# Optimization experiments

Measured on AMD Instinct MI355X. Metric: run time of the kernel, lower is better.

Reference implementation:

```python
import jax, jax.numpy as jnp
import numpy as np

H = 8      # num_heads
DH = 80    # head_dim = embed_dim // num_heads


def setup_inputs() -> dict:
    key = jax.random.key(0)
    ks = jax.random.split(key, 7)
    B, T, S = 8, 4096, 77
    hidden, embed, ctx = 640, 640, 768
    sc_h = 1.0 / np.sqrt(hidden)
    sc_c = 1.0 / np.sqrt(ctx)
    sc_e = 1.0 / np.sqrt(embed)
    return {
        "tokens": jax.random.normal(ks[0], (B, T, hidden), jnp.float32),
        "context": jax.random.normal(ks[1], (B, S, ctx), jnp.float32),
        "Wq": jax.random.normal(ks[2], (hidden, embed), jnp.float32) * sc_h,
        "Wk": jax.random.normal(ks[3], (ctx, embed), jnp.float32) * sc_c,
        "Wv": jax.random.normal(ks[4], (ctx, embed), jnp.float32) * sc_c,
        "Wo": jax.random.normal(ks[5], (embed, hidden), jnp.float32) * sc_e,
        "bo": jnp.zeros((hidden,), jnp.float32),
    }


def reference(tokens, context, Wq, Wk, Wv, Wo, bo):
    B, T, _ = tokens.shape
    S = context.shape[1]
    Q = (tokens @ Wq).reshape(B, T, H, DH)    # B T H D
    K = (context @ Wk).reshape(B, S, H, DH)   # B S H D
    V = (context @ Wv).reshape(B, S, H, DH)
    scores = jnp.einsum('bthd,bshd->bhts', Q, K) / jnp.sqrt(jnp.float32(DH))
    attn = jax.nn.softmax(scores, axis=-1)    # B H T S
    ctx_vecs = jnp.einsum('bhts,bshd->bthd', attn, V).reshape(B, T, H * DH)
    return ctx_vecs @ Wo + bo
```

## Files before the change

### kernel.cpp

```cpp
#include <hip/hip_runtime.h>
#include <hip/hip_bf16.h>
#include <hip/hip_fp16.h>

typedef __attribute__((ext_vector_type(4))) float f32x4;
typedef __attribute__((ext_vector_type(8))) _Float16 f16x8;
typedef __attribute__((ext_vector_type(8))) unsigned short u16x8;

__device__ __forceinline__ unsigned short f2h(float f) {
    _Float16 h = (_Float16)f;
    return __builtin_bit_cast(unsigned short, h);
}

#define GLOAD_LDS16(gp, lp) __builtin_amdgcn_global_load_lds( \
    (const __attribute__((address_space(1))) void*)(gp), \
    (__attribute__((address_space(3))) void*)(lp), 16, 0, 0)
#define PRIO1() __builtin_amdgcn_s_setprio(1)
#define PRIO0() __builtin_amdgcn_s_setprio(0)

__global__ void cvt_kernel(const float* __restrict__ in, ushort* __restrict__ out, int n4) {
    int stride = gridDim.x * blockDim.x;
    for (int i = blockIdx.x * blockDim.x + threadIdx.x; i < n4; i += stride) {
        float4 v = ((const float4*)in)[i];
        ushort4 o;
        o.x = f2h(v.x); o.y = f2h(v.y); o.z = f2h(v.z); o.w = f2h(v.w);
        ((ushort4*)out)[i] = o;
    }
}

__global__ void transpose_cvt2(const float* __restrict__ Wk, const float* __restrict__ Wv,
                               ushort* __restrict__ WkvT) {
    __shared__ float tile[32][33];
    const int z = blockIdx.z;
    const float* src = z ? Wv : Wk;
    ushort* dst = WkvT + (size_t)z * 640 * 768;
    const int R = 768, C = 640;
    int tx = threadIdx.x, ty = threadIdx.y;
    int c = blockIdx.x * 32 + tx;
    int r0 = blockIdx.y * 32;
#pragma unroll
    for (int i = ty; i < 32; i += 8) {
        int r = r0 + i;
        tile[i][tx] = (r < R && c < C) ? src[(size_t)r * C + c] : 0.f;
    }
    __syncthreads();
    int rr = r0 + tx;
    int c0 = blockIdx.x * 32;
#pragma unroll
    for (int i = ty; i < 32; i += 8) {
        int cc = c0 + i;
        if (cc < C && rr < R) dst[(size_t)cc * R + rr] = f2h(tile[tx][i]);
    }
}

__global__ void pack_wfrag(const float* __restrict__ W, ushort* __restrict__ WF) {
    int g = blockIdx.x * 256 + threadIdx.x;
    if (g >= 51200) return;
    int lane = g & 63;
    int fi = (g >> 6) % 10;
    int kt = ((g >> 6) / 10) % 10;
    int h  = (g >> 6) / 100;
    int ni = fi >> 1, kk = fi & 1;
    int n  = h * 80 + ni * 16 + (lane & 15);
    int k0 = kt * 64 + kk * 32 + (lane >> 4) * 8;
    u16x8 o;
#pragma unroll
    for (int e = 0; e < 8; ++e) o[e] = f2h(W[(size_t)(k0 + e) * 640 + n]);
    *(u16x8*)&WF[(size_t)g * 8] = o;
}

__global__ void pack_kvfrag(const ushort* __restrict__ KVb,
                            ushort* __restrict__ KF, ushort* __restrict__ VF) {
    int g = blockIdx.x * 256 + threadIdx.x;
    if (g >= 61440) return;
    int lane = g & 63;
    int fi = (g >> 6) % 15;
    int bh = (g >> 6) / 15;
    int b = bh >> 3, h = bh & 7;
    int ni = fi / 3, kk = fi % 3;
    int l15 = lane & 15, lhi = lane >> 4;
    int sr = ni * 16 + l15; if (sr > 76) sr = 76;
    int d0 = kk * 32 + lhi * 8;
    u16x8 ko, vo;
#pragma unroll
    for (int e = 0; e < 8; ++e)
        ko[e] = KVb[((size_t)b * 77 + sr) * 1280 + h * 80 + d0 + e];
    int dv = ni * 16 + l15;
    int s0 = kk * 32 + lhi * 8;
#pragma unroll
    for (int e = 0; e < 8; ++e) {
        int s = s0 + e;
        vo[e] = (s < 77) ? KVb[((size_t)b * 77 + s) * 1280 + 640 + h * 80 + dv] : (ushort)0;
    }
    *(u16x8*)&KF[(size_t)g * 8] = ko;
    *(u16x8*)&VF[(size_t)g * 8] = vo;
}

template<int OUT_F16, int HAS_BIAS>
__global__ __launch_bounds__(256) void gemm_bt(
    const ushort* __restrict__ A, const ushort* __restrict__ Bt,
    void* __restrict__ C, const float* __restrict__ bias,
    int M, int N, int K)
{
    __shared__ ushort As[128 * 64];
    __shared__ ushort Bs[128 * 64];
    const int tid = threadIdx.x;
    const int lane = tid & 63;
    const int w = tid >> 6;
    const int wr = (w >> 1) * 64, wc = (w & 1) * 64;
    const int m0 = blockIdx.x * 128, n0 = blockIdx.y * 128;
    const int l15 = lane & 15, lhi = lane >> 4;

    f32x4 acc[4][4] = {};

    for (int k0 = 0; k0 < K; k0 += 64) {
        __syncthreads();
#pragma unroll
        for (int i = 0; i < 4; ++i) {
            int c = i * 256 + tid;
            int m = m0 + (c >> 3);
            if (m > M - 1) m = M - 1;
            GLOAD_LDS16(A + (size_t)m * K + k0 + (c & 7) * 8, &As[c * 8]);
        }
#pragma unroll
        for (int i = 0; i < 4; ++i) {
            int c = i * 256 + tid;
            GLOAD_LDS16(Bt + (size_t)(n0 + (c >> 3)) * K + k0 + (c & 7) * 8, &Bs[c * 8]);
        }
        __syncthreads();
#pragma unroll
        for (int kk = 0; kk < 2; ++kk) {
            f16x8 af[4], bfr[4];
#pragma unroll
            for (int mi = 0; mi < 4; ++mi)
                af[mi] = *(const f16x8*)&As[(wr + mi * 16 + l15) * 64 + kk * 32 + lhi * 8];
#pragma unroll
            for (int ni = 0; ni < 4; ++ni)
                bfr[ni] = *(const f16x8*)&Bs[(wc + ni * 16 + l15) * 64 + kk * 32 + lhi * 8];
#pragma unroll
            for (int mi = 0; mi < 4; ++mi)
#pragma unroll
                for (int ni = 0; ni < 4; ++ni)
                    acc[mi][ni] = __builtin_amdgcn_mfma_f32_16x16x32_f16(
                        af[mi], bfr[ni], acc[mi][ni], 0, 0, 0);
        }
    }

#pragma unroll
    for (int mi = 0; mi < 4; ++mi)
#pragma unroll
        for (int ni = 0; ni < 4; ++ni)
#pragma unroll
            for (int r = 0; r < 4; ++r) {
                int row = m0 + wr + mi * 16 + lhi * 4 + r;
                int col = n0 + wc + ni * 16 + l15;
                if (row < M) {
                    float v = acc[mi][ni][r];
                    if (HAS_BIAS) v += bias[col];
                    if (OUT_F16) ((ushort*)C)[(size_t)row * N + col] = f2h(v);
                    else         ((float*)C)[(size_t)row * N + col] = v;
                }
            }
}

__global__ __launch_bounds__(1024, 1) void fused_attn(
    const float* __restrict__ tokens, const ushort* __restrict__ WqF,
    const ushort* __restrict__ KF, const ushort* __restrict__ VF,
    const ushort* __restrict__ WoF, const float* __restrict__ bo,
    float* __restrict__ out)
{
    __shared__ __align__(16) ushort lds[40960];
    const int tid = threadIdx.x;
    const int lane = tid & 63;
    const int w = tid >> 6;
    const int h = w & 7;
    const int rh = w >> 3;
    const int l15 = lane & 15, lhi = lane >> 4;
    const int tt = blockIdx.x, b = blockIdx.y;
    const size_t rowbase = (size_t)b * 4096 + (size_t)tt * 64;

    const ushort* WqFb = WqF + (size_t)h * 10 * 5120;
    const ushort* WoFb = WoF + (size_t)h * 10 * 5120;
    const ushort* KFb  = KF + (size_t)(b * 8 + h) * 15 * 512;
    const ushort* VFb  = VF + (size_t)(b * 8 + h) * 15 * 512;

    const bool stager = tid < 512;
    const int rs = (tid & 511) >> 3;
    const int ss = tid & 7;
    const int ds = rs * 64 + (ss ^ (rs & 7)) * 8;

#define STAGE_LOAD(C, A0, B0) do { \
    if (stager) { \
        const float* p_ = tokens + (rowbase + rs) * 640 + (C) * 64 + ss * 8; \
        A0 = ((const float4*)p_)[0]; B0 = ((const float4*)p_)[1]; \
    } \
} while (0)
#define STAGE_WRITE(BUF, A0, B0) do { \
    if (stager) { \
        u16x8 o_; \
        o_[0]=f2h(A0.x); o_[1]=f2h(A0.y); o_[2]=f2h(A0.z); o_[3]=f2h(A0.w); \
        o_[4]=f2h(B0.x); o_[5]=f2h(B0.y); o_[6]=f2h(B0.z); o_[7]=f2h(B0.w); \
        *(u16x8*)&lds[(BUF) * 4096 + ds] = o_; \
    } \
} while (0)

    {
        float4 a0, b0;
        STAGE_LOAD(0, a0, b0);
        STAGE_WRITE(0, a0, b0);
    }
    f16x8 PE[5], PO[5];
#pragma unroll
    for (int f = 0; f < 5; ++f)
        PE[f] = *(const f16x8*)(WqFb + (f * 2) * 512 + lane * 8);
    __syncthreads();

    f32x4 acc[2][5];
#define ZACC() do { \
    _Pragma("unroll") for (int i_ = 0; i_ < 2; ++i_) \
    _Pragma("unroll") for (int j_ = 0; j_ < 5; ++j_) \
        acc[i_][j_] = (f32x4){0.f, 0.f, 0.f, 0.f}; \
} while (0)

#define MHALF(PC, PN, WB, CURB, RSTR, SBASE, KK, NKT, NKK, DOPF) do { \
    if (DOPF) { \
        _Pragma("unroll") for (int f = 0; f < 5; ++f) \
            (PN)[f] = *(const f16x8*)((WB) + (size_t)(NKT) * 5120 + (f * 2 + (NKK)) * 512 + lane * 8); \
    } \
    PRIO1(); \
    _Pragma("unroll") for (int mi = 0; mi < 2; ++mi) { \
        int row_ = rh * 32 + mi * 16 + l15; \
        f16x8 a_ = *(const f16x8*)&lds[(CURB) + row_ * (RSTR) + ((SBASE) + (((KK) * 4 + lhi) ^ (row_ & 7))) * 8]; \
        _Pragma("unroll") for (int ni = 0; ni < 5; ++ni) \
            acc[mi][ni] = __builtin_amdgcn_mfma_f32_16x16x32_f16(a_, (PC)[ni], acc[mi][ni], 0, 0, 0); \
    } \
    PRIO0(); \
} while (0)

    ZACC();
    for (int kt = 0; kt < 10; ++kt) {
        const int curb = (kt & 1) * 4096;
        float4 a0, b0;
        if (kt < 9) STAGE_LOAD(kt + 1, a0, b0);
        MHALF(PE, PO, WqFb, curb, 64, 0, 0, kt, 1, 1);
        MHALF(PO, PE, WqFb, curb, 64, 0, 1, kt + 1, 0, kt < 9);
        if (kt < 9) STAGE_WRITE((kt + 1) & 1, a0, b0);
        __syncthreads();
    }

    const int qoff = w * 2560;
#pragma unroll
    for (int mi = 0; mi < 2; ++mi)
#pragma unroll
        for (int ni = 0; ni < 5; ++ni)
#pragma unroll
            for (int r = 0; r < 4; ++r)
                lds[qoff + (mi*16 + lhi*4 + r)*80 + ni*16 + l15] = f2h(acc[mi][ni][r]);
    __builtin_amdgcn_sched_barrier(0);

    const f16x8 zf = {};
#define ATT_KK(PC, PN, FB, KK, NKK, DOPF) do { \
    if (DOPF) { \
        _Pragma("unroll") for (int f = 0; f < 5; ++f) \
            (PN)[f] = *(const f16x8*)((FB) + (f * 3 + (NKK)) * 512 + lane * 8); \
    } \
    const int kcol = ((KK) < 2) ? ((KK)*32 + lhi*8) : (64 + (lhi & 1)*8); \
    PRIO1(); \
    _Pragma("unroll") for (int mi = 0; mi < 2; ++mi) { \
        f16x8 aq_ = *(const f16x8*)&lds[qoff + (mi*16 + l15)*80 + kcol]; \
        if ((KK) == 2 && lhi >= 2) aq_ = zf; \
        _Pragma("unroll") for (int ni = 0; ni < 5; ++ni) \
            acc[mi][ni] = __builtin_amdgcn_mfma_f32_16x16x32_f16(aq_, (PC)[ni], acc[mi][ni], 0, 0, 0); \
    } \
    PRIO0(); \
} while (0)

    ZACC();
#pragma unroll
    for (int f = 0; f < 5; ++f)
        PE[f] = *(const f16x8*)(KFb + (f * 3) * 512 + lane * 8);
    ATT_KK(PE, PO, KFb, 0, 1, 1);
    ATT_KK(PO, PE, KFb, 1, 2, 1);
    ATT_KK(PE, PO, KFb, 2, 0, 0);
    __builtin_amdgcn_sched_barrier(0);

    const float sc = 0.11180339887498949f;
#pragma unroll
    for (int mi = 0; mi < 2; ++mi)
#pragma unroll
        for (int r = 0; r < 4; ++r) {
            float v0 = acc[mi][0][r]*sc, v1 = acc[mi][1][r]*sc, v2 = acc[mi][2][r]*sc,
                  v3 = acc[mi][3][r]*sc, v4 = acc[mi][4][r]*sc;
            bool ok4 = l15 < 13;
            float mx = fmaxf(fmaxf(v0, v1), fmaxf(v2, v3));
            if (ok4) mx = fmaxf(mx, v4);
#pragma unroll
            for (int off = 1; off < 16; off <<= 1) mx = fmaxf(mx, __shfl_xor(mx, off, 16));
            float p0 = __expf(v0-mx), p1 = __expf(v1-mx), p2 = __expf(v2-mx), p3 = __expf(v3-mx);
            float p4 = ok4 ? __expf(v4-mx) : 0.f;
            float sm = p0+p1+p2+p3+p4;
#pragma unroll
            for (int off = 1; off < 16; off <<= 1) sm += __shfl_xor(sm, off, 16);
            float inv = 1.f / sm;
            int row = mi*16 + lhi*4 + r;
            lds[qoff + row*80 + 0*16 + l15] = f2h(p0*inv);
            lds[qoff + row*80 + 1*16 + l15] = f2h(p1*inv);
            lds[qoff + row*80 + 2*16 + l15] = f2h(p2*inv);
            lds[qoff + row*80 + 3*16 + l15] = f2h(p3*inv);
            lds[qoff + row*80 + 4*16 + l15] = f2h(p4*inv);
        }
    __builtin_amdgcn_sched_barrier(0);

    ZACC();
#pragma unroll
    for (int f = 0; f < 5; ++f)
        PE[f] = *(const f16x8*)(VFb + (f * 3) * 512 + lane * 8);
    ATT_KK(PE, PO, VFb, 0, 1, 1);
    ATT_KK(PO, PE, VFb, 1, 2, 1);
    ATT_KK(PE, PO, VFb, 2, 0, 0);
#undef ATT_KK
    __syncthreads();

#pragma unroll
    for (int mi = 0; mi < 2; ++mi)
#pragma unroll
        for (int ni = 0; ni < 5; ++ni)
#pragma unroll
            for (int r = 0; r < 4; ++r) {
                int row = rh*32 + mi*16 + lhi*4 + r;
                int col = h*80 + ni*16 + l15;
                int slot = col >> 3;
                int phys = (slot & ~7) | ((slot ^ row) & 7);
                lds[row*640 + phys*8 + (col & 7)] = f2h(acc[mi][ni][r]);
            }
    __syncthreads();

    ZACC();
#pragma unroll
    for (int f = 0; f < 5; ++f)
        PE[f] = *(const f16x8*)(WoFb + (f * 2) * 512 + lane * 8);
    for (int kt = 0; kt < 10; ++kt) {
        MHALF(PE, PO, WoFb, 0, 640, kt * 8, 0, kt, 1, 1);
        MHALF(PO, PE, WoFb, 0, 640, kt * 8, 1, kt + 1, 0, kt < 9);
    }
#undef MHALF
#undef ZACC

#pragma unroll
    for (int ni = 0; ni < 5; ++ni) {
        int col = h*80 + ni*16 + l15;
        float bvl = bo[col];
#pragma unroll
        for (int mi = 0; mi < 2; ++mi)
#pragma unroll
            for (int r = 0; r < 4; ++r)
                out[(rowbase + rh*32 + mi*16 + lhi*4 + r) * 640 + col] = acc[mi][ni][r] + bvl;
    }
#undef STAGE_LOAD
#undef STAGE_WRITE
}

extern "C" void kernel_launch(void* const* d_in, const int* in_sizes, int n_in,
                              void* d_out, int out_size, void* d_ws, size_t ws_size,
                              hipStream_t stream) {
    (void)in_sizes; (void)n_in; (void)out_size; (void)ws_size;
    const float* tokens  = (const float*)d_in[0];
    const float* context = (const float*)d_in[1];
    const float* Wq = (const float*)d_in[2];
    const float* Wk = (const float*)d_in[3];
    const float* Wv = (const float*)d_in[4];
    const float* Wo = (const float*)d_in[5];
    const float* bo = (const float*)d_in[6];
    float* out = (float*)d_out;

    ushort* ws   = (ushort*)d_ws;
    ushort* ctx16 = ws;
    ushort* WkvT = ctx16 + (size_t)616 * 768;
    ushort* KVb  = WkvT + (size_t)1280 * 768;
    ushort* WqF  = KVb  + (size_t)616 * 1280;
    ushort* WoF  = WqF  + (size_t)640 * 640;
    ushort* KF   = WoF  + (size_t)640 * 640;
    ushort* VF   = KF   + (size_t)61440 * 8;

    cvt_kernel<<<462, 256, 0, stream>>>(context, ctx16, 616 * 768 / 4);
    transpose_cvt2<<<dim3(20, 24, 2), dim3(32, 8), 0, stream>>>(Wk, Wv, WkvT);
    pack_wfrag<<<200, 256, 0, stream>>>(Wq, WqF);
    pack_wfrag<<<200, 256, 0, stream>>>(Wo, WoF);
    gemm_bt<1, 0><<<dim3(5, 10), 256, 0, stream>>>(ctx16, WkvT, KVb, nullptr, 616, 1280, 768);
    pack_kvfrag<<<240, 256, 0, stream>>>(KVb, KF, VF);
    fused_attn<<<dim3(64, 8), 1024, 0, stream>>>(tokens, WqF, KF, VF, WoF, bo, out);
}
```

Before: 135.4 us.

## Restructure fused attention to 512 threads with LDS-staged weight prefetch pipeline

The fused attention kernel moves from 1024 threads (two waves per head, 32 rows each) to 512 threads (one wave per head, 64 rows), so each wave reuses every loaded weight fragment across twice as many rows. Wq and Wo fragments are now streamed into LDS with global_load_lds using triple/double buffering and explicit vmcnt waits, replacing register prefetch. Token staging is deepened to two chunks ahead. The two weight-packing launches are merged into one 2D launch. The cost is double the LDS footprint and a larger accumulator set per wave, which may limit occupancy to one block per CU despite the launch bounds of 2.

```diff
diff --git a/kernel.cpp b/kernel.cpp
--- a/kernel.cpp
+++ b/kernel.cpp
@@ -16,6 +16,8 @@
     (__attribute__((address_space(3))) void*)(lp), 16, 0, 0)
 #define PRIO1() __builtin_amdgcn_s_setprio(1)
 #define PRIO0() __builtin_amdgcn_s_setprio(0)
+#define WAITVM(LIT) do { asm volatile("s_waitcnt vmcnt(" #LIT ")" ::: "memory"); \
+                         __builtin_amdgcn_sched_barrier(0); } while (0)
 
 __global__ void cvt_kernel(const float* __restrict__ in, ushort* __restrict__ out, int n4) {
     int stride = gridDim.x * blockDim.x;
@@ -52,9 +54,12 @@
     }
 }
 
-__global__ void pack_wfrag(const float* __restrict__ W, ushort* __restrict__ WF) {
+__global__ void pack_wfrag2(const float* __restrict__ Wq, const float* __restrict__ Wo,
+                            ushort* __restrict__ WqF, ushort* __restrict__ WoF) {
     int g = blockIdx.x * 256 + threadIdx.x;
     if (g >= 51200) return;
+    const float* W = blockIdx.y ? Wo : Wq;
+    ushort* WF = blockIdx.y ? WoF : WqF;
     int lane = g & 63;
     int fi = (g >> 6) % 10;
     int kt = ((g >> 6) / 10) % 10;
@@ -162,94 +167,128 @@
             }
 }
 
-__global__ __launch_bounds__(1024, 1) void fused_attn(
+__global__ __launch_bounds__(512, 2) void fused_attn(
     const float* __restrict__ tokens, const ushort* __restrict__ WqF,
     const ushort* __restrict__ KF, const ushort* __restrict__ VF,
     const ushort* __restrict__ WoF, const float* __restrict__ bo,
     float* __restrict__ out)
 {
-    __shared__ __align__(16) ushort lds[40960];
+    __shared__ __align__(16) ushort lds[81920];
     const int tid = threadIdx.x;
     const int lane = tid & 63;
     const int w = tid >> 6;
-    const int h = w & 7;
-    const int rh = w >> 3;
     const int l15 = lane & 15, lhi = lane >> 4;
     const int tt = blockIdx.x, b = blockIdx.y;
     const size_t rowbase = (size_t)b * 4096 + (size_t)tt * 64;
 
-    const ushort* WqFb = WqF + (size_t)h * 10 * 5120;
-    const ushort* WoFb = WoF + (size_t)h * 10 * 5120;
-    const ushort* KFb  = KF + (size_t)(b * 8 + h) * 15 * 512;
-    const ushort* VFb  = VF + (size_t)(b * 8 + h) * 15 * 512;
-
-    const bool stager = tid < 512;
-    const int rs = (tid & 511) >> 3;
-    const int ss = tid & 7;
-    const int ds = rs * 64 + (ss ^ (rs & 7)) * 8;
+    const ushort* WqFb = WqF + (size_t)w * 10 * 5120;
+    const ushort* WoFb = WoF + (size_t)w * 10 * 5120;
+    const ushort* KFb  = KF + (size_t)(b * 8 + w) * 15 * 512;
+    const ushort* VFb  = VF + (size_t)(b * 8 + w) * 15 * 512;
+    const int qstrip = 8192 + w * 7680;
+    const int ostrip = 40960 + w * 5120;
+
+    const int srow = tid >> 3;
+    const int sc8  = tid & 7;
+    const int sphys = (sc8 ^ (srow & 7)) * 8;
 
 #define STAGE_LOAD(C, A0, B0) do { \
-    if (stager) { \
-        const float* p_ = tokens + (rowbase + rs) * 640 + (C) * 64 + ss * 8; \
-        A0 = ((const float4*)p_)[0]; B0 = ((const float4*)p_)[1]; \
-    } \
+    const float* p_ = tokens + (rowbase + srow) * 640 + (C) * 64 + sc8 * 8; \
+    A0 = ((const float4*)p_)[0]; B0 = ((const float4*)p_)[1]; \
 } while (0)
 #define STAGE_WRITE(BUF, A0, B0) do { \
-    if (stager) { \
-        u16x8 o_; \
-        o_[0]=f2h(A0.x); o_[1]=f2h(A0.y); o_[2]=f2h(A0.z); o_[3]=f2h(A0.w); \
-        o_[4]=f2h(B0.x); o_[5]=f2h(B0.y); o_[6]=f2h(B0.z); o_[7]=f2h(B0.w); \
-        *(u16x8*)&lds[(BUF) * 4096 + ds] = o_; \
-    } \
-} while (0)
-
-    {
-        float4 a0, b0;
-        STAGE_LOAD(0, a0, b0);
-        STAGE_WRITE(0, a0, b0);
-    }
-    f16x8 PE[5], PO[5];
-#pragma unroll
-    for (int f = 0; f < 5; ++f)
-        PE[f] = *(const f16x8*)(WqFb + (f * 2) * 512 + lane * 8);
-    __syncthreads();
-
-    f32x4 acc[2][5];
+    u16x8 o_; \
+    o_[0]=f2h(A0.x); o_[1]=f2h(A0.y); o_[2]=f2h(A0.z); o_[3]=f2h(A0.w); \
+    o_[4]=f2h(B0.x); o_[5]=f2h(B0.y); o_[6]=f2h(B0.z); o_[7]=f2h(B0.w); \
+    *(u16x8*)&lds[(BUF) * 4096 + srow * 64 + sphys] = o_; \
+} while (0)
+
+#define GLOADB_Q(HX) do { \
+    if ((HX) <= 19) { \
+        const ushort* s_ = WqFb + ((HX) >> 1) * 5120 + ((HX) & 1) * 512 + lane * 8; \
+        _Pragma("unroll") for (int f_ = 0; f_ < 5; ++f_) \
+            GLOAD_LDS16(s_ + f_ * 1024, &lds[qstrip + ((HX) % 3) * 2560 + f_ * 512]); \
+    } \
+} while (0)
+#define GLOADB_O(HX) do { \
+    if ((HX) <= 19) { \
+        const ushort* s_ = WoFb + ((HX) >> 1) * 5120 + ((HX) & 1) * 512 + lane * 8; \
+        _Pragma("unroll") for (int f_ = 0; f_ < 5; ++f_) \
+            GLOAD_LDS16(s_ + f_ * 1024, &lds[ostrip + ((HX) & 1) * 2560 + f_ * 512]); \
+    } \
+} while (0)
+
+    f32x4 acc[4][5];
 #define ZACC() do { \
-    _Pragma("unroll") for (int i_ = 0; i_ < 2; ++i_) \
+    _Pragma("unroll") for (int i_ = 0; i_ < 4; ++i_) \
     _Pragma("unroll") for (int j_ = 0; j_ < 5; ++j_) \
         acc[i_][j_] = (f32x4){0.f, 0.f, 0.f, 0.f}; \
 } while (0)
 
-#define MHALF(PC, PN, WB, CURB, RSTR, SBASE, KK, NKT, NKK, DOPF) do { \
-    if (DOPF) { \
-        _Pragma("unroll") for (int f = 0; f < 5; ++f) \
-            (PN)[f] = *(const f16x8*)((WB) + (size_t)(NKT) * 5120 + (f * 2 + (NKK)) * 512 + lane * 8); \
-    } \
+#define MFMA_Q(KT, KK) do { \
+    f16x8 bf_[5]; \
+    _Pragma("unroll") for (int ni = 0; ni < 5; ++ni) \
+        bf_[ni] = *(const f16x8*)&lds[qstrip + ((2*(KT)+(KK)) % 3) * 2560 + ni * 512 + lane * 8]; \
     PRIO1(); \
-    _Pragma("unroll") for (int mi = 0; mi < 2; ++mi) { \
-        int row_ = rh * 32 + mi * 16 + l15; \
-        f16x8 a_ = *(const f16x8*)&lds[(CURB) + row_ * (RSTR) + ((SBASE) + (((KK) * 4 + lhi) ^ (row_ & 7))) * 8]; \
+    _Pragma("unroll") for (int mi = 0; mi < 4; ++mi) { \
+        int row_ = mi * 16 + l15; \
+        f16x8 a_ = *(const f16x8*)&lds[((KT) & 1) * 4096 + row_ * 64 + (((KK)*4 + lhi) ^ (row_ & 7)) * 8]; \
         _Pragma("unroll") for (int ni = 0; ni < 5; ++ni) \
-            acc[mi][ni] = __builtin_amdgcn_mfma_f32_16x16x32_f16(a_, (PC)[ni], acc[mi][ni], 0, 0, 0); \
+            acc[mi][ni] = __builtin_amdgcn_mfma_f32_16x16x32_f16(a_, bf_[ni], acc[mi][ni], 0, 0, 0); \
     } \
     PRIO0(); \
 } while (0)
+#define MFMA_O(HX) do { \
+    f16x8 bf_[5]; \
+    _Pragma("unroll") for (int ni = 0; ni < 5; ++ni) \
+        bf_[ni] = *(const f16x8*)&lds[ostrip + ((HX) & 1) * 2560 + ni * 512 + lane * 8]; \
+    PRIO1(); \
+    _Pragma("unroll") for (int mi = 0; mi < 4; ++mi) { \
+        int row_ = mi * 16 + l15; \
+        f16x8 a_ = *(const f16x8*)&lds[row_ * 640 + (((HX) >> 1) * 8 + ((((HX) & 1)*4 + lhi) ^ (row_ & 7))) * 8]; \
+        _Pragma("unroll") for (int ni = 0; ni < 5; ++ni) \
+            acc[mi][ni] = __builtin_amdgcn_mfma_f32_16x16x32_f16(a_, bf_[ni], acc[mi][ni], 0, 0, 0); \
+    } \
+    PRIO0(); \
+} while (0)
+
+#define QKT(KT, WA, WB, LA, LB, WRA, WRB) do { \
+    if ((KT) < 8) STAGE_LOAD((KT) + 2, LA, LB); \
+    GLOADB_Q(2*(KT) + 2); \
+    WAITVM(WA); \
+    if ((KT) < 9) STAGE_WRITE(((KT)+1) & 1, WRA, WRB); \
+    MFMA_Q(KT, 0); \
+    GLOADB_Q(2*(KT) + 3); \
+    WAITVM(WB); \
+    MFMA_Q(KT, 1); \
+    __syncthreads(); \
+} while (0)
+
+    float4 sA0, sB0, sA1, sB1;
+    STAGE_LOAD(0, sA0, sB0);
+    STAGE_LOAD(1, sA1, sB1);
+    GLOADB_Q(0);
+    GLOADB_Q(1);
+    WAITVM(10);
+    STAGE_WRITE(0, sA0, sB0);
+    __syncthreads();
 
     ZACC();
-    for (int kt = 0; kt < 10; ++kt) {
-        const int curb = (kt & 1) * 4096;
-        float4 a0, b0;
-        if (kt < 9) STAGE_LOAD(kt + 1, a0, b0);
-        MHALF(PE, PO, WqFb, curb, 64, 0, 0, kt, 1, 1);
-        MHALF(PO, PE, WqFb, curb, 64, 0, 1, kt + 1, 0, kt < 9);
-        if (kt < 9) STAGE_WRITE((kt + 1) & 1, a0, b0);
-        __syncthreads();
-    }
-
-    const int qoff = w * 2560;
-#pragma unroll
-    for (int mi = 0; mi < 2; ++mi)
+    QKT(0, 10, 10, sA0, sB0, sA1, sB1);
+    QKT(1, 10, 10, sA1, sB1, sA0, sB0);
+    QKT(2, 10, 10, sA0, sB0, sA1, sB1);
+    QKT(3, 10, 10, sA1, sB1, sA0, sB0);
+    QKT(4, 10, 10, sA0, sB0, sA1, sB1);
+    QKT(5, 10, 10, sA1, sB1, sA0, sB0);
+    QKT(6, 10, 10, sA0, sB0, sA1, sB1);
+    QKT(7, 10, 10, sA1, sB1, sA0, sB0);
+    QKT(8, 10, 10, sA0, sB0, sA1, sB1);
+    QKT(9,  5,  0, sA0, sB0, sA1, sB1);
+#undef QKT
+
+    const int qoff = w * 5120;
+#pragma unroll
+    for (int mi = 0; mi < 4; ++mi)
 #pragma unroll
         for (int ni = 0; ni < 5; ++ni)
 #pragma unroll
@@ -258,6 +297,7 @@
     __builtin_amdgcn_sched_barrier(0);
 
     const f16x8 zf = {};
+    f16x8 PE[5], PO[5];
 #define ATT_KK(PC, PN, FB, KK, NKK, DOPF) do { \
     if (DOPF) { \
         _Pragma("unroll") for (int f = 0; f < 5; ++f) \
@@ -265,7 +305,7 @@
     } \
     const int kcol = ((KK) < 2) ? ((KK)*32 + lhi*8) : (64 + (lhi & 1)*8); \
     PRIO1(); \
-    _Pragma("unroll") for (int mi = 0; mi < 2; ++mi) { \
+    _Pragma("unroll") for (int mi = 0; mi < 4; ++mi) { \
         f16x8 aq_ = *(const f16x8*)&lds[qoff + (mi*16 + l15)*80 + kcol]; \
         if ((KK) == 2 && lhi >= 2) aq_ = zf; \
         _Pragma("unroll") for (int ni = 0; ni < 5; ++ni) \
@@ -285,7 +325,7 @@
 
     const float sc = 0.11180339887498949f;
 #pragma unroll
-    for (int mi = 0; mi < 2; ++mi)
+    for (int mi = 0; mi < 4; ++mi)
 #pragma unroll
         for (int r = 0; r < 4; ++r) {
             float v0 = acc[mi][0][r]*sc, v1 = acc[mi][1][r]*sc, v2 = acc[mi][2][r]*sc,
@@ -318,16 +358,18 @@
     ATT_KK(PO, PE, VFb, 1, 2, 1);
     ATT_KK(PE, PO, VFb, 2, 0, 0);
 #undef ATT_KK
+
+    GLOADB_O(0);
     __syncthreads();
 
 #pragma unroll
-    for (int mi = 0; mi < 2; ++mi)
+    for (int mi = 0; mi < 4; ++mi)
 #pragma unroll
         for (int ni = 0; ni < 5; ++ni)
 #pragma unroll
             for (int r = 0; r < 4; ++r) {
-                int row = rh*32 + mi*16 + lhi*4 + r;
-                int col = h*80 + ni*16 + l15;
+                int row = mi*16 + lhi*4 + r;
+                int col = w*80 + ni*16 + l15;
                 int slot = col >> 3;
                 int phys = (slot & ~7) | ((slot ^ row) & 7);
                 lds[row*640 + phys*8 + (col & 7)] = f2h(acc[mi][ni][r]);
@@ -335,28 +377,30 @@
     __syncthreads();
 
     ZACC();
-#pragma unroll
-    for (int f = 0; f < 5; ++f)
-        PE[f] = *(const f16x8*)(WoFb + (f * 2) * 512 + lane * 8);
-    for (int kt = 0; kt < 10; ++kt) {
-        MHALF(PE, PO, WoFb, 0, 640, kt * 8, 0, kt, 1, 1);
-        MHALF(PO, PE, WoFb, 0, 640, kt * 8, 1, kt + 1, 0, kt < 9);
-    }
-#undef MHALF
-#undef ZACC
+#define OH(HX, W) do { GLOADB_O((HX) + 1); WAITVM(W); MFMA_O(HX); } while (0)
+    OH(0, 5);  OH(1, 5);  OH(2, 5);  OH(3, 5);  OH(4, 5);
+    OH(5, 5);  OH(6, 5);  OH(7, 5);  OH(8, 5);  OH(9, 5);
+    OH(10, 5); OH(11, 5); OH(12, 5); OH(13, 5); OH(14, 5);
+    OH(15, 5); OH(16, 5); OH(17, 5); OH(18, 5); OH(19, 0);
+#undef OH
 
 #pragma unroll
     for (int ni = 0; ni < 5; ++ni) {
-        int col = h*80 + ni*16 + l15;
+        int col = w*80 + ni*16 + l15;
         float bvl = bo[col];
 #pragma unroll
-        for (int mi = 0; mi < 2; ++mi)
+        for (int mi = 0; mi < 4; ++mi)
 #pragma unroll
             for (int r = 0; r < 4; ++r)
-                out[(rowbase + rh*32 + mi*16 + lhi*4 + r) * 640 + col] = acc[mi][ni][r] + bvl;
+                out[(rowbase + mi*16 + lhi*4 + r) * 640 + col] = acc[mi][ni][r] + bvl;
     }
 #undef STAGE_LOAD
 #undef STAGE_WRITE
+#undef GLOADB_Q
+#undef GLOADB_O
+#undef MFMA_Q
+#undef MFMA_O
+#undef ZACC
 }
 
 extern "C" void kernel_launch(void* const* d_in, const int* in_sizes, int n_in,
@@ -383,9 +427,8 @@
 
     cvt_kernel<<<462, 256, 0, stream>>>(context, ctx16, 616 * 768 / 4);
     transpose_cvt2<<<dim3(20, 24, 2), dim3(32, 8), 0, stream>>>(Wk, Wv, WkvT);
-    pack_wfrag<<<200, 256, 0, stream>>>(Wq, WqF);
-    pack_wfrag<<<200, 256, 0, stream>>>(Wo, WoF);
+    pack_wfrag2<<<dim3(200, 2), 256, 0, stream>>>(Wq, Wo, WqF, WoF);
     gemm_bt<1, 0><<<dim3(5, 10), 256, 0, stream>>>(ctx16, WkvT, KVb, nullptr, 616, 1280, 768);
     pack_kvfrag<<<240, 256, 0, stream>>>(KVb, KF, VF);
-    fused_attn<<<dim3(64, 8), 1024, 0, stream>>>(tokens, WqF, KF, VF, WoF, bo, out);
-}
+    fused_attn<<<dim3(64, 8), 512, 0, stream>>>(tokens, WqF, KF, VF, WoF, bo, out);
+}
```

After: 127.2 us. -6.0%, faster.
